# Kernel optimization log

Measured on AMD Instinct MI355X. Metric: run time of the kernel, lower is better.

## Reference

```python
import jax, jax.numpy as jnp
import numpy as np

N_NODES = 50000
N_EDGES = 600000
D_IN = 128
DIM = 128
N_REL = 3
N_LAYERS = 2


def setup_inputs() -> dict:
    key = jax.random.key(0)
    ks = jax.random.split(key, 10)
    s = 1.0 / np.sqrt(DIM)
    x = jax.random.normal(ks[0], (N_NODES, D_IN), dtype=jnp.float32)
    edge_index = jax.random.randint(ks[1], (2, N_EDGES), 0, N_NODES)
    edge_type = jax.random.randint(ks[2], (N_EDGES,), 0, N_REL)
    edge_weight = jax.random.uniform(ks[3], (N_EDGES,), dtype=jnp.float32)
    # stacked per-layer parameters (layer dims are uniform since D_IN == DIM)
    w_rel = jax.random.normal(ks[4], (N_LAYERS, N_REL, DIM, DIM), dtype=jnp.float32) * s
    w_root = jax.random.normal(ks[5], (N_LAYERS, DIM, DIM), dtype=jnp.float32) * s
    b_conv = jnp.zeros((N_LAYERS, DIM), dtype=jnp.float32)
    w_skip = jax.random.normal(ks[6], (N_LAYERS, D_IN, DIM), dtype=jnp.float32) * s
    b_skip = jnp.zeros((N_LAYERS, DIM), dtype=jnp.float32)
    return {"x": x, "edge_index": edge_index, "edge_type": edge_type,
            "edge_weight": edge_weight, "w_rel": w_rel, "w_root": w_root,
            "b_conv": b_conv, "w_skip": w_skip, "b_skip": b_skip}


def reference(x, edge_index, edge_type, edge_weight, w_rel, w_root, b_conv, w_skip, b_skip):
    n = x.shape[0]
    src, dst = edge_index[0], edge_index[1]
    h = x
    for l in range(w_rel.shape[0]):  # small fixed layer loop (2)
        skip = x @ w_skip[l] + b_skip[l]                      # [N, dim]
        # per-relation transform of all nodes: [R, N, dim] (cheap GEMMs),
        # avoids materializing a per-edge [E, d, d] weight gather
        hr = jnp.einsum('nd,rde->rne', h, w_rel[l])
        msgs = hr[edge_type, src] * edge_weight[:, None]      # [E, dim] gather
        agg = jax.ops.segment_sum(msgs, dst, num_segments=n)  # scatter-add
        h = agg + h @ w_root[l] + b_conv[l] + skip            # conv + skip residual
    return h
```

## Files before the change

### kernel.cpp

```cpp
#include <hip/hip_runtime.h>


#define DIM 128

typedef short short8 __attribute__((ext_vector_type(8)));
typedef float f32x4 __attribute__((ext_vector_type(4)));

__device__ __forceinline__ unsigned short f2bf(float f) {
    unsigned u = __float_as_uint(f);
    unsigned r = (u + 0x7FFFu + ((u >> 16) & 1u)) >> 16;
    return (unsigned short)r;
}
__device__ __forceinline__ float bflo(unsigned p) { return __uint_as_float(p << 16); }
__device__ __forceinline__ float bfhi(unsigned p) { return __uint_as_float(p & 0xFFFF0000u); }

__device__ __forceinline__ int xcc_id() {
    int x;
    asm volatile("s_getreg_b32 %0, hwreg(HW_REG_XCC_ID)" : "=s"(x));
    return x & 7;
}

__global__ void zero_kernel(int4* __restrict__ p, int n4) {
    int i = blockIdx.x * 256 + threadIdx.x;
    if (i < n4) p[i] = make_int4(0, 0, 0, 0);
}

#define K2_CONVB 2048
#define K2_PREPB 256
#define K2_CNTB  512

__device__ void conv_body(const float* __restrict__ in, unsigned short* __restrict__ ob,
                          int n8, int bid) {
    for (int i = bid * 256 + threadIdx.x; i < n8; i += K2_CONVB * 256) {
        const float4* ip = reinterpret_cast<const float4*>(in) + (size_t)i * 2;
        float4 v0 = ip[0], v1 = ip[1];
        uint4 o;
        o.x = (unsigned)f2bf(v0.x) | ((unsigned)f2bf(v0.y) << 16);
        o.y = (unsigned)f2bf(v0.z) | ((unsigned)f2bf(v0.w) << 16);
        o.z = (unsigned)f2bf(v1.x) | ((unsigned)f2bf(v1.y) << 16);
        o.w = (unsigned)f2bf(v1.z) | ((unsigned)f2bf(v1.w) << 16);
        reinterpret_cast<uint4*>(ob)[i] = o;
    }
}

__device__ void prep_body(const float* __restrict__ w_rel, const float* __restrict__ w_root,
                          const float* __restrict__ w_skip, unsigned short* __restrict__ WTf,
                          int bid) {
    for (int i = bid * 256 + threadIdx.x; i < 2 * 5 * DIM * DIM; i += K2_PREPB * 256) {
        int j    = i & 7;
        int lane = (i >> 3) & 63;
        int ks   = (i >> 9) & 3;
        int n    = (i >> 11) & 7;
        int s    = (i >> 14) % 5;
        int l    = i / (5 * DIM * DIM);
        int col = n * 16 + (lane & 15);
        int k   = ks * 32 + (lane >> 4) * 8 + j;
        float v;
        if (s < 3)       v = w_rel[(((size_t)l * 3 + s) * DIM + k) * DIM + col];
        else if (s == 3) {
            v = w_root[((size_t)l * DIM + k) * DIM + col];
            if (l == 0) v += w_skip[((size_t)k) * DIM + col];
        } else           v = w_skip[((size_t)l * DIM + k) * DIM + col];
        WTf[i] = f2bf(v);
    }
}

__device__ void count_body(const int* __restrict__ dst, int* __restrict__ counts8,
                           unsigned short* __restrict__ rank, int E, int N, int bid) {
    int* cp = counts8 + (size_t)xcc_id() * N;
    unsigned tag = (unsigned)xcc_id() << 13;
    int t = threadIdx.x;
    for (int base = bid * 1024; base < E; base += K2_CNTB * 1024) {
        int i0 = base + t, i1 = i0 + 256, i2 = i0 + 512, i3 = i0 + 768;
        int d0 = (i0 < E) ? dst[i0] : -1;
        int d1 = (i1 < E) ? dst[i1] : -1;
        int d2 = (i2 < E) ? dst[i2] : -1;
        int d3 = (i3 < E) ? dst[i3] : -1;
        int r0 = (d0 >= 0) ? atomicAdd(&cp[d0], 1) : 0;
        int r1 = (d1 >= 0) ? atomicAdd(&cp[d1], 1) : 0;
        int r2 = (d2 >= 0) ? atomicAdd(&cp[d2], 1) : 0;
        int r3 = (d3 >= 0) ? atomicAdd(&cp[d3], 1) : 0;
        if (d0 >= 0) rank[i0] = (unsigned short)(r0 | tag);
        if (d1 >= 0) rank[i1] = (unsigned short)(r1 | tag);
        if (d2 >= 0) rank[i2] = (unsigned short)(r2 | tag);
        if (d3 >= 0) rank[i3] = (unsigned short)(r3 | tag);
    }
}

__global__ __launch_bounds__(256) void fat_prep(
    const float* __restrict__ x, unsigned short* __restrict__ xb, int n8,
    const float* __restrict__ w_rel, const float* __restrict__ w_root,
    const float* __restrict__ w_skip, unsigned short* __restrict__ WTf,
    const int* __restrict__ dst, int* __restrict__ counts8,
    unsigned short* __restrict__ rank, int E, int N) {
    int b = blockIdx.x;
    if (b < K2_CONVB)                 conv_body(x, xb, n8, b);
    else if (b < K2_CONVB + K2_PREPB) prep_body(w_rel, w_root, w_skip, WTf, b - K2_CONVB);
    else                              count_body(dst, counts8, rank, E, N, b - K2_CONVB - K2_PREPB);
}

__global__ void bsum_kernel(const int* __restrict__ counts8, int* __restrict__ bsums, int n) {
    int t = threadIdx.x;
    int i = blockIdx.x * 256 + t;
    int v = 0;
    if (i < n) {
        #pragma unroll
        for (int p = 0; p < 8; ++p) v += counts8[(size_t)p * n + i];
    }
    for (int d = 32; d; d >>= 1) v += __shfl_down(v, d);
    __shared__ int ws[4];
    if ((t & 63) == 0) ws[t >> 6] = v;
    __syncthreads();
    if (t == 0) bsums[blockIdx.x] = ws[0] + ws[1] + ws[2] + ws[3];
}

__global__ void bscan_kernel(const int* __restrict__ bsums, int* __restrict__ bpre, int nblk) {
    __shared__ int s[256];
    int t = threadIdx.x;
    int v = (t < nblk) ? bsums[t] : 0;
    s[t] = v;
    __syncthreads();
    for (int d = 1; d < 256; d <<= 1) {
        int u = (t >= d) ? s[t - d] : 0;
        __syncthreads();
        s[t] += u;
        __syncthreads();
    }
    bpre[t] = s[t] - v;
}

__global__ void scan_final(const int* __restrict__ counts8, const int* __restrict__ bpre,
                           int* __restrict__ offsets, int* __restrict__ pos0,
                           int n, int E) {
    __shared__ int s[256];
    int t = threadIdx.x;
    int i = blockIdx.x * 256 + t;
    int c[8];
    int v = 0;
    if (i < n) {
        #pragma unroll
        for (int p = 0; p < 8; ++p) { c[p] = counts8[(size_t)p * n + i]; v += c[p]; }
    }
    s[t] = v;
    __syncthreads();
    for (int d = 1; d < 256; d <<= 1) {
        int u = (t >= d) ? s[t - d] : 0;
        __syncthreads();
        s[t] += u;
        __syncthreads();
    }
    int ex = s[t] - v + bpre[blockIdx.x];
    if (i < n) {
        offsets[i] = ex;
        int run = ex;
        #pragma unroll
        for (int p = 0; p < 8; ++p) { pos0[(size_t)p * n + i] = run; run += c[p]; }
    }
    if (i == 0) offsets[n] = E;
}

template<bool HAS_SKIP>
__device__ void gemm_body(
    int bid,
    const unsigned short* __restrict__ Ab, const unsigned short* __restrict__ Xb,
    const unsigned short* __restrict__ WTf,
    const float* __restrict__ bconv, const float* __restrict__ bskip,
    unsigned short* __restrict__ hr, void* __restrict__ outp, int M) {
    constexpr int NF = HAS_SKIP ? 40 : 32;
    __shared__ unsigned short stile[4][32][136];
    int t = threadIdx.x, lane = t & 63, wid = t >> 6;
    int lrow = lane & 15, lhi = lane >> 4;
    int r0 = bid * 128 + wid * 32;

    short8 af[2][4];
    #pragma unroll
    for (int rg = 0; rg < 2; ++rg) {
        int r = r0 + rg * 16 + lrow;
        const unsigned short* ap = Ab + (size_t)(r < M ? r : 0) * DIM + lhi * 8;
        #pragma unroll
        for (int ks = 0; ks < 4; ++ks)
            af[rg][ks] = *reinterpret_cast<const short8*>(ap + ks * 32);
    }
    short8 xf[2][4];
    f32x4 acc34[2][8];

    auto flush = [&](unsigned short* gbase) {
        #pragma unroll
        for (int j = 0; j < 8; ++j) {
            int lr = j * 4 + lhi;
            int lc = lrow * 8;
            int gr = r0 + lr;
            if (gr < M)
                *reinterpret_cast<uint4*>(gbase + (size_t)gr * DIM + lc) =
                    *reinterpret_cast<const uint4*>(&stile[wid][lr][lc]);
        }
    };

    short8 b0[4], b1[4];
    auto loadB = [&](int fi, short8* bb) {
        const unsigned short* p = WTf + ((size_t)fi * 4 * 64 + lane) * 8;
        #pragma unroll
        for (int ks = 0; ks < 4; ++ks)
            bb[ks] = *reinterpret_cast<const short8*>(p + ks * 512);
    };
    loadB(0, b0);
    #pragma unroll
    for (int fi = 0; fi < NF; ++fi) {
        short8* bc = (fi & 1) ? b1 : b0;
        short8* bn = (fi & 1) ? b0 : b1;
        if (fi + 1 < NF) loadB(fi + 1, bn);
        const int slot = fi >> 3, n = fi & 7;
        const int col = n * 16 + lrow;
        if (HAS_SKIP && slot == 3 && n == 0) {
            #pragma unroll
            for (int rg = 0; rg < 2; ++rg) {
                int r = r0 + rg * 16 + lrow;
                const unsigned short* xp = Xb + (size_t)(r < M ? r : 0) * DIM + lhi * 8;
                #pragma unroll
                for (int ks = 0; ks < 4; ++ks)
                    xf[rg][ks] = *reinterpret_cast<const short8*>(xp + ks * 32);
            }
        }
        if (slot < 3) {
            f32x4 a0 = {0.f, 0.f, 0.f, 0.f}, a1 = {0.f, 0.f, 0.f, 0.f};
            #pragma unroll
            for (int ks = 0; ks < 4; ++ks) {
                a0 = __builtin_amdgcn_mfma_f32_16x16x32_bf16(af[0][ks], bc[ks], a0, 0, 0, 0);
                a1 = __builtin_amdgcn_mfma_f32_16x16x32_bf16(af[1][ks], bc[ks], a1, 0, 0, 0);
            }
            #pragma unroll
            for (int rg = 0; rg < 2; ++rg) {
                f32x4& aa = rg ? a1 : a0;
                #pragma unroll
                for (int i2 = 0; i2 < 4; ++i2)
                    stile[wid][rg * 16 + lhi * 4 + i2][col] = f2bf(aa[i2]);
            }
            if (n == 7) flush(hr + (size_t)slot * M * DIM);
        } else if (!HAS_SKIP) {
            f32x4 a0 = {0.f, 0.f, 0.f, 0.f}, a1 = {0.f, 0.f, 0.f, 0.f};
            #pragma unroll
            for (int ks = 0; ks < 4; ++ks) {
                a0 = __builtin_amdgcn_mfma_f32_16x16x32_bf16(af[0][ks], bc[ks], a0, 0, 0, 0);
                a1 = __builtin_amdgcn_mfma_f32_16x16x32_bf16(af[1][ks], bc[ks], a1, 0, 0, 0);
            }
            float bb = bconv[col] + bskip[col];
            #pragma unroll
            for (int rg = 0; rg < 2; ++rg) {
                f32x4& aa = rg ? a1 : a0;
                #pragma unroll
                for (int i2 = 0; i2 < 4; ++i2)
                    stile[wid][rg * 16 + lhi * 4 + i2][col] = f2bf(aa[i2] + bb);
            }
            if (n == 7) flush((unsigned short*)outp);
        } else if (slot == 3) {
            f32x4 z = {0.f, 0.f, 0.f, 0.f};
            acc34[0][n] = z; acc34[1][n] = z;
            #pragma unroll
            for (int ks = 0; ks < 4; ++ks) {
                acc34[0][n] = __builtin_amdgcn_mfma_f32_16x16x32_bf16(af[0][ks], bc[ks], acc34[0][n], 0, 0, 0);
                acc34[1][n] = __builtin_amdgcn_mfma_f32_16x16x32_bf16(af[1][ks], bc[ks], acc34[1][n], 0, 0, 0);
            }
        } else {
            #pragma unroll
            for (int ks = 0; ks < 4; ++ks) {
                acc34[0][n] = __builtin_amdgcn_mfma_f32_16x16x32_bf16(xf[0][ks], bc[ks], acc34[0][n], 0, 0, 0);
                acc34[1][n] = __builtin_amdgcn_mfma_f32_16x16x32_bf16(xf[1][ks], bc[ks], acc34[1][n], 0, 0, 0);
            }
            float bb = bconv[col] + bskip[col];
            float* op = (float*)outp;
            #pragma unroll
            for (int rg = 0; rg < 2; ++rg) {
                #pragma unroll
                for (int i2 = 0; i2 < 4; ++i2) {
                    int r = r0 + rg * 16 + lhi * 4 + i2;
                    if (r < M) op[(size_t)r * DIM + col] = acc34[rg][n][i2] + bb;
                }
            }
        }
    }
}

#define K6_SCTB 512

__device__ void scatter_body(const int* __restrict__ src, const int* __restrict__ dst,
                             const int* __restrict__ etype, const float* __restrict__ ew,
                             const int* __restrict__ pos0,
                             const unsigned short* __restrict__ rank,
                             unsigned* __restrict__ csr, int E, int N, int bid) {
    for (int i = bid * 256 + threadIdx.x; i < E; i += K6_SCTB * 256) {
        int d = dst[i];
        unsigned rk = rank[i];
        int part = rk >> 13;
        int p = pos0[(size_t)part * N + d] + (rk & 0x1FFF);
        unsigned wq = (unsigned)__float2uint_rn(ew[i] * 16383.0f);
        csr[p] = (unsigned)src[i] | ((unsigned)etype[i] << 16) | (wq << 18);
    }
}

__global__ __launch_bounds__(256) void gemm0_scatter(
    const unsigned short* __restrict__ Ab, const unsigned short* __restrict__ WTf,
    const float* __restrict__ bconv, const float* __restrict__ bskip,
    unsigned short* __restrict__ hr, unsigned short* __restrict__ h1, int M, int GB,
    const int* __restrict__ src, const int* __restrict__ dst,
    const int* __restrict__ etype, const float* __restrict__ ew,
    const int* __restrict__ pos0, const unsigned short* __restrict__ rank,
    unsigned* __restrict__ csr, int E) {
    int b = blockIdx.x;
    if (b < GB) gemm_body<false>(b, Ab, nullptr, WTf, bconv, bskip, hr, h1, M);
    else        scatter_body(src, dst, etype, ew, pos0, rank, csr, E, M, b - GB);
}

__global__ __launch_bounds__(256) void gemm1_kernel(
    const unsigned short* __restrict__ Ab, const unsigned short* __restrict__ Xb,
    const unsigned short* __restrict__ WTf,
    const float* __restrict__ bconv, const float* __restrict__ bskip,
    unsigned short* __restrict__ hr, float* __restrict__ outp, int M) {
    gemm_body<true>(blockIdx.x, Ab, Xb, WTf, bconv, bskip, hr, outp, M);
}

template<bool BF16IO>
__global__ __launch_bounds__(256) void agg_kernel(
    const unsigned short* __restrict__ hr, const unsigned* __restrict__ csr,
    const int* __restrict__ offsets, float* __restrict__ outf,
    unsigned short* __restrict__ outb, int N) {
    int t = threadIdx.x;
    int lane = t & 63;
    int v = blockIdx.x * 4 + (t >> 6);
    if (v >= N) return;
    int g = lane >> 4;
    int l16 = lane & 15;
    int beg = offsets[v], end = offsets[v + 1];

    float acc[8] = {0.f, 0.f, 0.f, 0.f, 0.f, 0.f, 0.f, 0.f};
    int i = beg + g;
    bool valid = i < end;
    unsigned st = valid ? csr[i] : 0u;
    while (__any(valid)) {
        int ni = i + 4;
        bool nv = ni < end;
        unsigned nst = nv ? csr[ni] : 0u;
        if (valid) {
            int srcn = st & 0xFFFF;
            int rel  = (st >> 16) & 3;
            float w  = (float)(st >> 18) * (1.0f / 16383.0f);
            const unsigned short* row = hr + ((size_t)rel * N + srcn) * DIM + l16 * 8;
            uint4 pv = *reinterpret_cast<const uint4*>(row);
            acc[0] += w * bflo(pv.x); acc[1] += w * bfhi(pv.x);
            acc[2] += w * bflo(pv.y); acc[3] += w * bfhi(pv.y);
            acc[4] += w * bflo(pv.z); acc[5] += w * bfhi(pv.z);
            acc[6] += w * bflo(pv.w); acc[7] += w * bfhi(pv.w);
        }
        i = ni; st = nst; valid = nv;
    }
    #pragma unroll
    for (int j = 0; j < 8; ++j) {
        acc[j] += __shfl_xor(acc[j], 16);
        acc[j] += __shfl_xor(acc[j], 32);
    }
    if (g == 0) {
        if (BF16IO) {
            unsigned short* op = outb + (size_t)v * DIM + l16 * 8;
            uint4 cur = *reinterpret_cast<const uint4*>(op);
            float r0 = bflo(cur.x) + acc[0], r1 = bfhi(cur.x) + acc[1];
            float r2 = bflo(cur.y) + acc[2], r3 = bfhi(cur.y) + acc[3];
            float r4 = bflo(cur.z) + acc[4], r5 = bfhi(cur.z) + acc[5];
            float r6 = bflo(cur.w) + acc[6], r7 = bfhi(cur.w) + acc[7];
            uint4 o;
            o.x = (unsigned)f2bf(r0) | ((unsigned)f2bf(r1) << 16);
            o.y = (unsigned)f2bf(r2) | ((unsigned)f2bf(r3) << 16);
            o.z = (unsigned)f2bf(r4) | ((unsigned)f2bf(r5) << 16);
            o.w = (unsigned)f2bf(r6) | ((unsigned)f2bf(r7) << 16);
            *reinterpret_cast<uint4*>(op) = o;
        } else {
            float* op = outf + (size_t)v * DIM + l16 * 8;
            float4 c0 = *reinterpret_cast<float4*>(op);
            float4 c1 = *reinterpret_cast<float4*>(op + 4);
            c0.x += acc[0]; c0.y += acc[1]; c0.z += acc[2]; c0.w += acc[3];
            c1.x += acc[4]; c1.y += acc[5]; c1.z += acc[6]; c1.w += acc[7];
            *reinterpret_cast<float4*>(op) = c0;
            *reinterpret_cast<float4*>(op + 4) = c1;
        }
    }
}

extern "C" void kernel_launch(void* const* d_in, const int* in_sizes, int n_in,
                              void* d_out, int out_size, void* d_ws, size_t ws_size,
                              hipStream_t stream) {
    const float* x       = (const float*)d_in[0];
    const int*   eidx    = (const int*)d_in[1];
    const int*   etype   = (const int*)d_in[2];
    const float* ew      = (const float*)d_in[3];
    const float* w_rel   = (const float*)d_in[4];
    const float* w_root  = (const float*)d_in[5];
    const float* b_conv  = (const float*)d_in[6];
    const float* w_skip  = (const float*)d_in[7];
    const float* b_skip  = (const float*)d_in[8];

    const int N = in_sizes[0] / DIM;
    const int E = in_sizes[3];
    const int* src = eidx;
    const int* dst = eidx + E;
    const int nblk = (N + 255) / 256;

    char* w = (char*)d_ws;
    unsigned short* WTf  = (unsigned short*)w;  w += (size_t)2 * 5 * DIM * DIM * 2;
    unsigned short* xb   = (unsigned short*)w;  w += (size_t)N * DIM * 2;
    unsigned short* hr   = (unsigned short*)w;  w += (size_t)3 * N * DIM * 2;
    unsigned short* h1   = (unsigned short*)w;  w += (size_t)N * DIM * 2;
    int* counts8         = (int*)w;             w += (size_t)8 * N * 4;
    int* pos0            = (int*)w;             w += (size_t)8 * N * 4;
    int* offsets         = (int*)w;             w += (size_t)(N + 4) * 4;
    int* bsums           = (int*)w;             w += (size_t)256 * 4;
    int* bpre            = (int*)w;             w += (size_t)256 * 4;
    unsigned short* rank = (unsigned short*)w;  w += (size_t)E * 2;
    unsigned* csr        = (unsigned*)w;        w += (size_t)E * 4;

    float* out = (float*)d_out;

    const int n8 = N * DIM / 8;
    zero_kernel<<<(8 * N / 4 + 255) / 256, 256, 0, stream>>>((int4*)counts8, 8 * N / 4);
    fat_prep<<<K2_CONVB + K2_PREPB + K2_CNTB, 256, 0, stream>>>(
        x, xb, n8, w_rel, w_root, w_skip, WTf, dst, counts8, rank, E, N);
    bsum_kernel<<<nblk, 256, 0, stream>>>(counts8, bsums, N);
    bscan_kernel<<<1, 256, 0, stream>>>(bsums, bpre, nblk);
    scan_final<<<nblk, 256, 0, stream>>>(counts8, bpre, offsets, pos0, N, E);

    int GB = (N + 127) / 128;
    int ablocks = (N + 3) / 4;
    gemm0_scatter<<<GB + K6_SCTB, 256, 0, stream>>>(
        xb, WTf, b_conv, b_skip, hr, h1, N, GB,
        src, dst, etype, ew, pos0, rank, csr, E);
    agg_kernel<true><<<ablocks, 256, 0, stream>>>(hr, csr, offsets, nullptr, h1, N);
    gemm1_kernel<<<GB, 256, 0, stream>>>(h1, xb, WTf + (size_t)5 * DIM * DIM,
                                         b_conv + DIM, b_skip + DIM, hr, out, N);
    agg_kernel<false><<<ablocks, 256, 0, stream>>>(hr, csr, offsets, out, nullptr, N);
}
```

Before: 160.6 us.

## Aggregate before transform: gather raw features per relation, then GEMM

Reorders each layer so that neighbour features are first summed per relation into a [N,3,128] bf16 buffer, and the relation weights are applied afterwards in a GEMM. This replaces the old path, which wrote and then gathered a 3xN per-relation transformed array. The root and skip terms are folded into the same GEMM accumulators. Gathered rows shrink from hr to the plain feature array, which is more cache friendly, but the aggregation kernel now holds three accumulator sets and writes a 3x wider output, and one extra kernel launch is added. The fat_prep block order is also changed so the counting blocks run first.

```diff
diff --git a/kernel.cpp b/kernel.cpp
--- a/kernel.cpp
+++ b/kernel.cpp
@@ -13,6 +13,7 @@
 }
 __device__ __forceinline__ float bflo(unsigned p) { return __uint_as_float(p << 16); }
 __device__ __forceinline__ float bfhi(unsigned p) { return __uint_as_float(p & 0xFFFF0000u); }
+__device__ __forceinline__ float bfu(unsigned short u) { return __uint_as_float((unsigned)u << 16); }
 
 __device__ __forceinline__ int xcc_id() {
     int x;
@@ -25,9 +26,9 @@
     if (i < n4) p[i] = make_int4(0, 0, 0, 0);
 }
 
+#define K2_CNTB  512
+#define K2_PREPB 256
 #define K2_CONVB 2048
-#define K2_PREPB 256
-#define K2_CNTB  512
 
 __device__ void conv_body(const float* __restrict__ in, unsigned short* __restrict__ ob,
                           int n8, int bid) {
@@ -94,9 +95,9 @@
     const int* __restrict__ dst, int* __restrict__ counts8,
     unsigned short* __restrict__ rank, int E, int N) {
     int b = blockIdx.x;
-    if (b < K2_CONVB)                 conv_body(x, xb, n8, b);
-    else if (b < K2_CONVB + K2_PREPB) prep_body(w_rel, w_root, w_skip, WTf, b - K2_CONVB);
-    else                              count_body(dst, counts8, rank, E, N, b - K2_CONVB - K2_PREPB);
+    if (b < K2_CNTB)                 count_body(dst, counts8, rank, E, N, b);
+    else if (b < K2_CNTB + K2_PREPB) prep_body(w_rel, w_root, w_skip, WTf, b - K2_CNTB);
+    else                             conv_body(x, xb, n8, b - K2_CNTB - K2_PREPB);
 }
 
 __global__ void bsum_kernel(const int* __restrict__ counts8, int* __restrict__ bsums, int n) {
@@ -159,14 +160,10 @@
     if (i == 0) offsets[n] = E;
 }
 
-template<bool HAS_SKIP>
-__device__ void gemm_body(
-    int bid,
-    const unsigned short* __restrict__ Ab, const unsigned short* __restrict__ Xb,
-    const unsigned short* __restrict__ WTf,
-    const float* __restrict__ bconv, const float* __restrict__ bskip,
-    unsigned short* __restrict__ hr, void* __restrict__ outp, int M) {
-    constexpr int NF = HAS_SKIP ? 40 : 32;
+__device__ void root0_body(int bid, const unsigned short* __restrict__ xb,
+                           const unsigned short* __restrict__ WTf0,
+                           const float* __restrict__ bconv, const float* __restrict__ bskip,
+                           unsigned short* __restrict__ h1, int M) {
     __shared__ unsigned short stile[4][32][136];
     int t = threadIdx.x, lane = t & 63, wid = t >> 6;
     int lrow = lane & 15, lhi = lane >> 4;
@@ -176,107 +173,46 @@
     #pragma unroll
     for (int rg = 0; rg < 2; ++rg) {
         int r = r0 + rg * 16 + lrow;
-        const unsigned short* ap = Ab + (size_t)(r < M ? r : 0) * DIM + lhi * 8;
+        const unsigned short* ap = xb + (size_t)(r < M ? r : 0) * DIM + lhi * 8;
         #pragma unroll
         for (int ks = 0; ks < 4; ++ks)
             af[rg][ks] = *reinterpret_cast<const short8*>(ap + ks * 32);
     }
-    short8 xf[2][4];
-    f32x4 acc34[2][8];
-
-    auto flush = [&](unsigned short* gbase) {
-        #pragma unroll
-        for (int j = 0; j < 8; ++j) {
-            int lr = j * 4 + lhi;
-            int lc = lrow * 8;
-            int gr = r0 + lr;
-            if (gr < M)
-                *reinterpret_cast<uint4*>(gbase + (size_t)gr * DIM + lc) =
-                    *reinterpret_cast<const uint4*>(&stile[wid][lr][lc]);
-        }
-    };
-
     short8 b0[4], b1[4];
-    auto loadB = [&](int fi, short8* bb) {
-        const unsigned short* p = WTf + ((size_t)fi * 4 * 64 + lane) * 8;
+    auto loadB = [&](int fia, short8* bb) {
+        const unsigned short* p = WTf0 + ((size_t)fia * 256 + lane) * 8;
         #pragma unroll
         for (int ks = 0; ks < 4; ++ks)
             bb[ks] = *reinterpret_cast<const short8*>(p + ks * 512);
     };
-    loadB(0, b0);
-    #pragma unroll
-    for (int fi = 0; fi < NF; ++fi) {
-        short8* bc = (fi & 1) ? b1 : b0;
-        short8* bn = (fi & 1) ? b0 : b1;
-        if (fi + 1 < NF) loadB(fi + 1, bn);
-        const int slot = fi >> 3, n = fi & 7;
-        const int col = n * 16 + lrow;
-        if (HAS_SKIP && slot == 3 && n == 0) {
-            #pragma unroll
-            for (int rg = 0; rg < 2; ++rg) {
-                int r = r0 + rg * 16 + lrow;
-                const unsigned short* xp = Xb + (size_t)(r < M ? r : 0) * DIM + lhi * 8;
-                #pragma unroll
-                for (int ks = 0; ks < 4; ++ks)
-                    xf[rg][ks] = *reinterpret_cast<const short8*>(xp + ks * 32);
-            }
-        }
-        if (slot < 3) {
-            f32x4 a0 = {0.f, 0.f, 0.f, 0.f}, a1 = {0.f, 0.f, 0.f, 0.f};
-            #pragma unroll
-            for (int ks = 0; ks < 4; ++ks) {
-                a0 = __builtin_amdgcn_mfma_f32_16x16x32_bf16(af[0][ks], bc[ks], a0, 0, 0, 0);
-                a1 = __builtin_amdgcn_mfma_f32_16x16x32_bf16(af[1][ks], bc[ks], a1, 0, 0, 0);
-            }
-            #pragma unroll
-            for (int rg = 0; rg < 2; ++rg) {
-                f32x4& aa = rg ? a1 : a0;
-                #pragma unroll
-                for (int i2 = 0; i2 < 4; ++i2)
-                    stile[wid][rg * 16 + lhi * 4 + i2][col] = f2bf(aa[i2]);
-            }
-            if (n == 7) flush(hr + (size_t)slot * M * DIM);
-        } else if (!HAS_SKIP) {
-            f32x4 a0 = {0.f, 0.f, 0.f, 0.f}, a1 = {0.f, 0.f, 0.f, 0.f};
-            #pragma unroll
-            for (int ks = 0; ks < 4; ++ks) {
-                a0 = __builtin_amdgcn_mfma_f32_16x16x32_bf16(af[0][ks], bc[ks], a0, 0, 0, 0);
-                a1 = __builtin_amdgcn_mfma_f32_16x16x32_bf16(af[1][ks], bc[ks], a1, 0, 0, 0);
-            }
-            float bb = bconv[col] + bskip[col];
-            #pragma unroll
-            for (int rg = 0; rg < 2; ++rg) {
-                f32x4& aa = rg ? a1 : a0;
-                #pragma unroll
-                for (int i2 = 0; i2 < 4; ++i2)
-                    stile[wid][rg * 16 + lhi * 4 + i2][col] = f2bf(aa[i2] + bb);
-            }
-            if (n == 7) flush((unsigned short*)outp);
-        } else if (slot == 3) {
-            f32x4 z = {0.f, 0.f, 0.f, 0.f};
-            acc34[0][n] = z; acc34[1][n] = z;
-            #pragma unroll
-            for (int ks = 0; ks < 4; ++ks) {
-                acc34[0][n] = __builtin_amdgcn_mfma_f32_16x16x32_bf16(af[0][ks], bc[ks], acc34[0][n], 0, 0, 0);
-                acc34[1][n] = __builtin_amdgcn_mfma_f32_16x16x32_bf16(af[1][ks], bc[ks], acc34[1][n], 0, 0, 0);
-            }
-        } else {
-            #pragma unroll
-            for (int ks = 0; ks < 4; ++ks) {
-                acc34[0][n] = __builtin_amdgcn_mfma_f32_16x16x32_bf16(xf[0][ks], bc[ks], acc34[0][n], 0, 0, 0);
-                acc34[1][n] = __builtin_amdgcn_mfma_f32_16x16x32_bf16(xf[1][ks], bc[ks], acc34[1][n], 0, 0, 0);
-            }
-            float bb = bconv[col] + bskip[col];
-            float* op = (float*)outp;
-            #pragma unroll
-            for (int rg = 0; rg < 2; ++rg) {
-                #pragma unroll
-                for (int i2 = 0; i2 < 4; ++i2) {
-                    int r = r0 + rg * 16 + lhi * 4 + i2;
-                    if (r < M) op[(size_t)r * DIM + col] = acc34[rg][n][i2] + bb;
-                }
-            }
-        }
+    loadB(24, b0);
+    #pragma unroll
+    for (int n = 0; n < 8; ++n) {
+        short8* bc = (n & 1) ? b1 : b0;
+        short8* bn = (n & 1) ? b0 : b1;
+        if (n + 1 < 8) loadB(24 + n + 1, bn);
+        f32x4 a0 = {0.f, 0.f, 0.f, 0.f}, a1 = {0.f, 0.f, 0.f, 0.f};
+        #pragma unroll
+        for (int ks = 0; ks < 4; ++ks) {
+            a0 = __builtin_amdgcn_mfma_f32_16x16x32_bf16(af[0][ks], bc[ks], a0, 0, 0, 0);
+            a1 = __builtin_amdgcn_mfma_f32_16x16x32_bf16(af[1][ks], bc[ks], a1, 0, 0, 0);
+        }
+        int col = n * 16 + lrow;
+        float bb = bconv[col] + bskip[col];
+        #pragma unroll
+        for (int rg = 0; rg < 2; ++rg) {
+            f32x4& aa = rg ? a1 : a0;
+            #pragma unroll
+            for (int i2 = 0; i2 < 4; ++i2)
+                stile[wid][rg * 16 + lhi * 4 + i2][col] = f2bf(aa[i2] + bb);
+        }
+    }
+    #pragma unroll
+    for (int j = 0; j < 8; ++j) {
+        int lr = j * 4 + lhi, gr = r0 + lr;
+        if (gr < M)
+            *reinterpret_cast<uint4*>(h1 + (size_t)gr * DIM + lrow * 8) =
+                *reinterpret_cast<const uint4*>(&stile[wid][lr][lrow * 8]);
     }
 }
 
@@ -297,41 +233,29 @@
     }
 }
 
-__global__ __launch_bounds__(256) void gemm0_scatter(
-    const unsigned short* __restrict__ Ab, const unsigned short* __restrict__ WTf,
+__global__ __launch_bounds__(256) void fat2_root_scatter(
+    const unsigned short* __restrict__ xb, const unsigned short* __restrict__ WTf0,
     const float* __restrict__ bconv, const float* __restrict__ bskip,
-    unsigned short* __restrict__ hr, unsigned short* __restrict__ h1, int M, int GB,
+    unsigned short* __restrict__ h1, int M, int GB,
     const int* __restrict__ src, const int* __restrict__ dst,
     const int* __restrict__ etype, const float* __restrict__ ew,
     const int* __restrict__ pos0, const unsigned short* __restrict__ rank,
     unsigned* __restrict__ csr, int E) {
     int b = blockIdx.x;
-    if (b < GB) gemm_body<false>(b, Ab, nullptr, WTf, bconv, bskip, hr, h1, M);
+    if (b < GB) root0_body(b, xb, WTf0, bconv, bskip, h1, M);
     else        scatter_body(src, dst, etype, ew, pos0, rank, csr, E, M, b - GB);
 }
 
-__global__ __launch_bounds__(256) void gemm1_kernel(
-    const unsigned short* __restrict__ Ab, const unsigned short* __restrict__ Xb,
-    const unsigned short* __restrict__ WTf,
-    const float* __restrict__ bconv, const float* __restrict__ bskip,
-    unsigned short* __restrict__ hr, float* __restrict__ outp, int M) {
-    gemm_body<true>(blockIdx.x, Ab, Xb, WTf, bconv, bskip, hr, outp, M);
-}
-
-template<bool BF16IO>
-__global__ __launch_bounds__(256) void agg_kernel(
-    const unsigned short* __restrict__ hr, const unsigned* __restrict__ csr,
-    const int* __restrict__ offsets, float* __restrict__ outf,
-    unsigned short* __restrict__ outb, int N) {
-    int t = threadIdx.x;
-    int lane = t & 63;
+__global__ __launch_bounds__(256) void agg2_kernel(
+    const unsigned short* __restrict__ pool, const unsigned* __restrict__ csr,
+    const int* __restrict__ offsets, unsigned short* __restrict__ aggbuf, int N) {
+    int t = threadIdx.x, lane = t & 63;
     int v = blockIdx.x * 4 + (t >> 6);
     if (v >= N) return;
-    int g = lane >> 4;
-    int l16 = lane & 15;
+    int g = lane >> 4, l16 = lane & 15;
     int beg = offsets[v], end = offsets[v + 1];
 
-    float acc[8] = {0.f, 0.f, 0.f, 0.f, 0.f, 0.f, 0.f, 0.f};
+    float a0[8] = {0,0,0,0,0,0,0,0}, a1[8] = {0,0,0,0,0,0,0,0}, a2[8] = {0,0,0,0,0,0,0,0};
     int i = beg + g;
     bool valid = i < end;
     unsigned st = valid ? csr[i] : 0u;
@@ -343,42 +267,180 @@
             int srcn = st & 0xFFFF;
             int rel  = (st >> 16) & 3;
             float w  = (float)(st >> 18) * (1.0f / 16383.0f);
-            const unsigned short* row = hr + ((size_t)rel * N + srcn) * DIM + l16 * 8;
+            const unsigned short* row = pool + (size_t)srcn * DIM + l16 * 8;
             uint4 pv = *reinterpret_cast<const uint4*>(row);
-            acc[0] += w * bflo(pv.x); acc[1] += w * bfhi(pv.x);
-            acc[2] += w * bflo(pv.y); acc[3] += w * bfhi(pv.y);
-            acc[4] += w * bflo(pv.z); acc[5] += w * bfhi(pv.z);
-            acc[6] += w * bflo(pv.w); acc[7] += w * bfhi(pv.w);
+            float f[8];
+            f[0] = bflo(pv.x); f[1] = bfhi(pv.x); f[2] = bflo(pv.y); f[3] = bfhi(pv.y);
+            f[4] = bflo(pv.z); f[5] = bfhi(pv.z); f[6] = bflo(pv.w); f[7] = bfhi(pv.w);
+            float w0 = (rel == 0) ? w : 0.f;
+            float w1 = (rel == 1) ? w : 0.f;
+            float w2 = (rel == 2) ? w : 0.f;
+            #pragma unroll
+            for (int j = 0; j < 8; ++j) {
+                a0[j] += w0 * f[j];
+                a1[j] += w1 * f[j];
+                a2[j] += w2 * f[j];
+            }
         }
         i = ni; st = nst; valid = nv;
     }
     #pragma unroll
     for (int j = 0; j < 8; ++j) {
-        acc[j] += __shfl_xor(acc[j], 16);
-        acc[j] += __shfl_xor(acc[j], 32);
-    }
-    if (g == 0) {
-        if (BF16IO) {
-            unsigned short* op = outb + (size_t)v * DIM + l16 * 8;
-            uint4 cur = *reinterpret_cast<const uint4*>(op);
-            float r0 = bflo(cur.x) + acc[0], r1 = bfhi(cur.x) + acc[1];
-            float r2 = bflo(cur.y) + acc[2], r3 = bfhi(cur.y) + acc[3];
-            float r4 = bflo(cur.z) + acc[4], r5 = bfhi(cur.z) + acc[5];
-            float r6 = bflo(cur.w) + acc[6], r7 = bfhi(cur.w) + acc[7];
-            uint4 o;
-            o.x = (unsigned)f2bf(r0) | ((unsigned)f2bf(r1) << 16);
-            o.y = (unsigned)f2bf(r2) | ((unsigned)f2bf(r3) << 16);
-            o.z = (unsigned)f2bf(r4) | ((unsigned)f2bf(r5) << 16);
-            o.w = (unsigned)f2bf(r6) | ((unsigned)f2bf(r7) << 16);
-            *reinterpret_cast<uint4*>(op) = o;
-        } else {
-            float* op = outf + (size_t)v * DIM + l16 * 8;
-            float4 c0 = *reinterpret_cast<float4*>(op);
-            float4 c1 = *reinterpret_cast<float4*>(op + 4);
-            c0.x += acc[0]; c0.y += acc[1]; c0.z += acc[2]; c0.w += acc[3];
-            c1.x += acc[4]; c1.y += acc[5]; c1.z += acc[6]; c1.w += acc[7];
-            *reinterpret_cast<float4*>(op) = c0;
-            *reinterpret_cast<float4*>(op + 4) = c1;
+        a0[j] += __shfl_xor(a0[j], 16); a0[j] += __shfl_xor(a0[j], 32);
+        a1[j] += __shfl_xor(a1[j], 16); a1[j] += __shfl_xor(a1[j], 32);
+        a2[j] += __shfl_xor(a2[j], 16); a2[j] += __shfl_xor(a2[j], 32);
+    }
+    if (g < 3) {
+        float o[8];
+        #pragma unroll
+        for (int j = 0; j < 8; ++j)
+            o[j] = (g == 0) ? a0[j] : ((g == 1) ? a1[j] : a2[j]);
+        unsigned short* op = aggbuf + (size_t)v * 384 + g * 128 + l16 * 8;
+        uint4 w4;
+        w4.x = (unsigned)f2bf(o[0]) | ((unsigned)f2bf(o[1]) << 16);
+        w4.y = (unsigned)f2bf(o[2]) | ((unsigned)f2bf(o[3]) << 16);
+        w4.z = (unsigned)f2bf(o[4]) | ((unsigned)f2bf(o[5]) << 16);
+        w4.w = (unsigned)f2bf(o[6]) | ((unsigned)f2bf(o[7]) << 16);
+        *reinterpret_cast<uint4*>(op) = w4;
+    }
+}
+
+__global__ __launch_bounds__(256) void gemm0_kernel(
+    const unsigned short* __restrict__ aggbuf, const unsigned short* __restrict__ WTf0,
+    unsigned short* __restrict__ h1, int M) {
+    __shared__ unsigned short stile[4][32][136];
+    int bid = blockIdx.x;
+    int t = threadIdx.x, lane = t & 63, wid = t >> 6;
+    int lrow = lane & 15, lhi = lane >> 4;
+    int r0 = bid * 128 + wid * 32;
+
+    #pragma unroll
+    for (int j = 0; j < 8; ++j) {
+        int lr = j * 4 + lhi, gr = r0 + lr;
+        if (gr < M)
+            *reinterpret_cast<uint4*>(&stile[wid][lr][lrow * 8]) =
+                *reinterpret_cast<const uint4*>(h1 + (size_t)gr * DIM + lrow * 8);
+    }
+    f32x4 acc[2][8];
+    #pragma unroll
+    for (int rg = 0; rg < 2; ++rg)
+        #pragma unroll
+        for (int n = 0; n < 8; ++n)
+            #pragma unroll
+            for (int i2 = 0; i2 < 4; ++i2)
+                acc[rg][n][i2] = bfu(stile[wid][rg * 16 + lhi * 4 + i2][n * 16 + lrow]);
+
+    short8 af[2][4];
+    short8 b0[4], b1[4];
+    auto loadB = [&](int fia, short8* bb) {
+        const unsigned short* p = WTf0 + ((size_t)fia * 256 + lane) * 8;
+        #pragma unroll
+        for (int ks = 0; ks < 4; ++ks)
+            bb[ks] = *reinterpret_cast<const short8*>(p + ks * 512);
+    };
+    loadB(0, b0);
+    #pragma unroll
+    for (int fi = 0; fi < 24; ++fi) {
+        short8* bc = (fi & 1) ? b1 : b0;
+        short8* bn = (fi & 1) ? b0 : b1;
+        if (fi + 1 < 24) loadB(fi + 1, bn);
+        const int slot = fi >> 3, n = fi & 7;
+        if (n == 0) {
+            #pragma unroll
+            for (int rg = 0; rg < 2; ++rg) {
+                int r = r0 + rg * 16 + lrow;
+                const unsigned short* ap = aggbuf + (size_t)(r < M ? r : 0) * 384
+                                           + slot * 128 + lhi * 8;
+                #pragma unroll
+                for (int ks = 0; ks < 4; ++ks)
+                    af[rg][ks] = *reinterpret_cast<const short8*>(ap + ks * 32);
+            }
+        }
+        #pragma unroll
+        for (int ks = 0; ks < 4; ++ks) {
+            acc[0][n] = __builtin_amdgcn_mfma_f32_16x16x32_bf16(af[0][ks], bc[ks], acc[0][n], 0, 0, 0);
+            acc[1][n] = __builtin_amdgcn_mfma_f32_16x16x32_bf16(af[1][ks], bc[ks], acc[1][n], 0, 0, 0);
+        }
+    }
+    #pragma unroll
+    for (int rg = 0; rg < 2; ++rg)
+        #pragma unroll
+        for (int n = 0; n < 8; ++n)
+            #pragma unroll
+            for (int i2 = 0; i2 < 4; ++i2)
+                stile[wid][rg * 16 + lhi * 4 + i2][n * 16 + lrow] = f2bf(acc[rg][n][i2]);
+    #pragma unroll
+    for (int j = 0; j < 8; ++j) {
+        int lr = j * 4 + lhi, gr = r0 + lr;
+        if (gr < M)
+            *reinterpret_cast<uint4*>(h1 + (size_t)gr * DIM + lrow * 8) =
+                *reinterpret_cast<const uint4*>(&stile[wid][lr][lrow * 8]);
+    }
+}
+
+__global__ __launch_bounds__(256) void gemm1_kernel(
+    const unsigned short* __restrict__ aggbuf, const unsigned short* __restrict__ h1,
+    const unsigned short* __restrict__ xb, const unsigned short* __restrict__ WTf1,
+    const float* __restrict__ bconv, const float* __restrict__ bskip,
+    float* __restrict__ out, int M) {
+    int bid = blockIdx.x;
+    int t = threadIdx.x, lane = t & 63, wid = t >> 6;
+    int lrow = lane & 15, lhi = lane >> 4;
+    int r0 = bid * 128 + wid * 32;
+
+    f32x4 acc[2][8];
+    #pragma unroll
+    for (int rg = 0; rg < 2; ++rg)
+        #pragma unroll
+        for (int n = 0; n < 8; ++n)
+            acc[rg][n] = f32x4{0.f, 0.f, 0.f, 0.f};
+
+    short8 af[2][4];
+    short8 b0[4], b1[4];
+    auto loadB = [&](int fia, short8* bb) {
+        const unsigned short* p = WTf1 + ((size_t)fia * 256 + lane) * 8;
+        #pragma unroll
+        for (int ks = 0; ks < 4; ++ks)
+            bb[ks] = *reinterpret_cast<const short8*>(p + ks * 512);
+    };
+    loadB(0, b0);
+    #pragma unroll
+    for (int fi = 0; fi < 40; ++fi) {
+        short8* bc = (fi & 1) ? b1 : b0;
+        short8* bn = (fi & 1) ? b0 : b1;
+        if (fi + 1 < 40) loadB(fi + 1, bn);
+        const int slot = fi >> 3, n = fi & 7;
+        if (n == 0) {
+            #pragma unroll
+            for (int rg = 0; rg < 2; ++rg) {
+                int r = r0 + rg * 16 + lrow;
+                int rc = r < M ? r : 0;
+                const unsigned short* ap;
+                if (slot < 3)      ap = aggbuf + (size_t)rc * 384 + slot * 128 + lhi * 8;
+                else if (slot == 3) ap = h1 + (size_t)rc * DIM + lhi * 8;
+                else                ap = xb + (size_t)rc * DIM + lhi * 8;
+                #pragma unroll
+                for (int ks = 0; ks < 4; ++ks)
+                    af[rg][ks] = *reinterpret_cast<const short8*>(ap + ks * 32);
+            }
+        }
+        #pragma unroll
+        for (int ks = 0; ks < 4; ++ks) {
+            acc[0][n] = __builtin_amdgcn_mfma_f32_16x16x32_bf16(af[0][ks], bc[ks], acc[0][n], 0, 0, 0);
+            acc[1][n] = __builtin_amdgcn_mfma_f32_16x16x32_bf16(af[1][ks], bc[ks], acc[1][n], 0, 0, 0);
+        }
+    }
+    #pragma unroll
+    for (int n = 0; n < 8; ++n) {
+        int col = n * 16 + lrow;
+        float bb = bconv[col] + bskip[col];
+        #pragma unroll
+        for (int rg = 0; rg < 2; ++rg) {
+            #pragma unroll
+            for (int i2 = 0; i2 < 4; ++i2) {
+                int r = r0 + rg * 16 + lhi * 4 + i2;
+                if (r < M) out[(size_t)r * DIM + col] = acc[rg][n][i2] + bb;
+            }
         }
     }
 }
@@ -405,7 +467,7 @@
     char* w = (char*)d_ws;
     unsigned short* WTf  = (unsigned short*)w;  w += (size_t)2 * 5 * DIM * DIM * 2;
     unsigned short* xb   = (unsigned short*)w;  w += (size_t)N * DIM * 2;
-    unsigned short* hr   = (unsigned short*)w;  w += (size_t)3 * N * DIM * 2;
+    unsigned short* agg  = (unsigned short*)w;  w += (size_t)N * 3 * DIM * 2;
     unsigned short* h1   = (unsigned short*)w;  w += (size_t)N * DIM * 2;
     int* counts8         = (int*)w;             w += (size_t)8 * N * 4;
     int* pos0            = (int*)w;             w += (size_t)8 * N * 4;
@@ -416,10 +478,11 @@
     unsigned* csr        = (unsigned*)w;        w += (size_t)E * 4;
 
     float* out = (float*)d_out;
+    const unsigned short* WTf1 = WTf + (size_t)5 * DIM * DIM;
 
     const int n8 = N * DIM / 8;
     zero_kernel<<<(8 * N / 4 + 255) / 256, 256, 0, stream>>>((int4*)counts8, 8 * N / 4);
-    fat_prep<<<K2_CONVB + K2_PREPB + K2_CNTB, 256, 0, stream>>>(
+    fat_prep<<<K2_CNTB + K2_PREPB + K2_CONVB, 256, 0, stream>>>(
         x, xb, n8, w_rel, w_root, w_skip, WTf, dst, counts8, rank, E, N);
     bsum_kernel<<<nblk, 256, 0, stream>>>(counts8, bsums, N);
     bscan_kernel<<<1, 256, 0, stream>>>(bsums, bpre, nblk);
@@ -427,11 +490,12 @@
 
     int GB = (N + 127) / 128;
     int ablocks = (N + 3) / 4;
-    gemm0_scatter<<<GB + K6_SCTB, 256, 0, stream>>>(
-        xb, WTf, b_conv, b_skip, hr, h1, N, GB,
+    fat2_root_scatter<<<GB + K6_SCTB, 256, 0, stream>>>(
+        xb, WTf, b_conv, b_skip, h1, N, GB,
         src, dst, etype, ew, pos0, rank, csr, E);
-    agg_kernel<true><<<ablocks, 256, 0, stream>>>(hr, csr, offsets, nullptr, h1, N);
-    gemm1_kernel<<<GB, 256, 0, stream>>>(h1, xb, WTf + (size_t)5 * DIM * DIM,
-                                         b_conv + DIM, b_skip + DIM, hr, out, N);
-    agg_kernel<false><<<ablocks, 256, 0, stream>>>(hr, csr, offsets, out, nullptr, N);
-}
+    agg2_kernel<<<ablocks, 256, 0, stream>>>(xb, csr, offsets, agg, N);
+    gemm0_kernel<<<GB, 256, 0, stream>>>(agg, WTf, h1, N);
+    agg2_kernel<<<ablocks, 256, 0, stream>>>(h1, csr, offsets, agg, N);
+    gemm1_kernel<<<GB, 256, 0, stream>>>(agg, h1, xb, WTf1,
+                                         b_conv + DIM, b_skip + DIM, out, N);
+}
```

New measurement: 205.0 us. 1.28x slower.

## Replace rank-based CSR build with atomic cursor scatter and unroll aggregation loads

Applied to the files above, without the earlier changes.

Removes the per-edge rank array and per-XCC position table. The count kernel now only increments histograms, and the scatter pass claims CSR slots with atomicAdd on a per-node cursor. The count pass is split out of the fused prep kernel into its own launch. The aggregation loop now processes two edges per iteration with both row gathers issued before accumulation, which raises memory-level parallelism. The trade-off is more global atomics during scatter and a nondeterministic order within each CSR segment, which changes float summation order. It also adds one extra kernel launch.

```diff
diff --git a/kernel.cpp b/kernel.cpp
--- a/kernel.cpp
+++ b/kernel.cpp
@@ -27,7 +27,6 @@
 
 #define K2_CONVB 2048
 #define K2_PREPB 256
-#define K2_CNTB  512
 
 __device__ void conv_body(const float* __restrict__ in, unsigned short* __restrict__ ob,
                           int n8, int bid) {
@@ -65,38 +64,28 @@
     }
 }
 
-__device__ void count_body(const int* __restrict__ dst, int* __restrict__ counts8,
-                           unsigned short* __restrict__ rank, int E, int N, int bid) {
-    int* cp = counts8 + (size_t)xcc_id() * N;
-    unsigned tag = (unsigned)xcc_id() << 13;
-    int t = threadIdx.x;
-    for (int base = bid * 1024; base < E; base += K2_CNTB * 1024) {
-        int i0 = base + t, i1 = i0 + 256, i2 = i0 + 512, i3 = i0 + 768;
-        int d0 = (i0 < E) ? dst[i0] : -1;
-        int d1 = (i1 < E) ? dst[i1] : -1;
-        int d2 = (i2 < E) ? dst[i2] : -1;
-        int d3 = (i3 < E) ? dst[i3] : -1;
-        int r0 = (d0 >= 0) ? atomicAdd(&cp[d0], 1) : 0;
-        int r1 = (d1 >= 0) ? atomicAdd(&cp[d1], 1) : 0;
-        int r2 = (d2 >= 0) ? atomicAdd(&cp[d2], 1) : 0;
-        int r3 = (d3 >= 0) ? atomicAdd(&cp[d3], 1) : 0;
-        if (d0 >= 0) rank[i0] = (unsigned short)(r0 | tag);
-        if (d1 >= 0) rank[i1] = (unsigned short)(r1 | tag);
-        if (d2 >= 0) rank[i2] = (unsigned short)(r2 | tag);
-        if (d3 >= 0) rank[i3] = (unsigned short)(r3 | tag);
-    }
-}
-
-__global__ __launch_bounds__(256) void fat_prep(
+__global__ __launch_bounds__(256) void convprep_kernel(
     const float* __restrict__ x, unsigned short* __restrict__ xb, int n8,
     const float* __restrict__ w_rel, const float* __restrict__ w_root,
-    const float* __restrict__ w_skip, unsigned short* __restrict__ WTf,
-    const int* __restrict__ dst, int* __restrict__ counts8,
-    unsigned short* __restrict__ rank, int E, int N) {
+    const float* __restrict__ w_skip, unsigned short* __restrict__ WTf) {
     int b = blockIdx.x;
-    if (b < K2_CONVB)                 conv_body(x, xb, n8, b);
-    else if (b < K2_CONVB + K2_PREPB) prep_body(w_rel, w_root, w_skip, WTf, b - K2_CONVB);
-    else                              count_body(dst, counts8, rank, E, N, b - K2_CONVB - K2_PREPB);
+    if (b < K2_CONVB) conv_body(x, xb, n8, b);
+    else              prep_body(w_rel, w_root, w_skip, WTf, b - K2_CONVB);
+}
+
+#define K_CNTB 512
+
+__global__ __launch_bounds__(256) void count_kernel(
+    const int* __restrict__ dst, int* __restrict__ counts8, int E, int N) {
+    int* cp = counts8 + (size_t)xcc_id() * N;
+    int bid = blockIdx.x, t = threadIdx.x;
+    for (int base = bid * 1024; base < E; base += K_CNTB * 1024) {
+        int i0 = base + t, i1 = i0 + 256, i2 = i0 + 512, i3 = i0 + 768;
+        if (i0 < E) atomicAdd(&cp[dst[i0]], 1);
+        if (i1 < E) atomicAdd(&cp[dst[i1]], 1);
+        if (i2 < E) atomicAdd(&cp[dst[i2]], 1);
+        if (i3 < E) atomicAdd(&cp[dst[i3]], 1);
+    }
 }
 
 __global__ void bsum_kernel(const int* __restrict__ counts8, int* __restrict__ bsums, int n) {
@@ -130,16 +119,15 @@
 }
 
 __global__ void scan_final(const int* __restrict__ counts8, const int* __restrict__ bpre,
-                           int* __restrict__ offsets, int* __restrict__ pos0,
+                           int* __restrict__ offsets, int* __restrict__ cursor,
                            int n, int E) {
     __shared__ int s[256];
     int t = threadIdx.x;
     int i = blockIdx.x * 256 + t;
-    int c[8];
     int v = 0;
     if (i < n) {
         #pragma unroll
-        for (int p = 0; p < 8; ++p) { c[p] = counts8[(size_t)p * n + i]; v += c[p]; }
+        for (int p = 0; p < 8; ++p) v += counts8[(size_t)p * n + i];
     }
     s[t] = v;
     __syncthreads();
@@ -150,12 +138,7 @@
         __syncthreads();
     }
     int ex = s[t] - v + bpre[blockIdx.x];
-    if (i < n) {
-        offsets[i] = ex;
-        int run = ex;
-        #pragma unroll
-        for (int p = 0; p < 8; ++p) { pos0[(size_t)p * n + i] = run; run += c[p]; }
-    }
+    if (i < n) { offsets[i] = ex; cursor[i] = ex; }
     if (i == 0) offsets[n] = E;
 }
 
@@ -284,14 +267,11 @@
 
 __device__ void scatter_body(const int* __restrict__ src, const int* __restrict__ dst,
                              const int* __restrict__ etype, const float* __restrict__ ew,
-                             const int* __restrict__ pos0,
-                             const unsigned short* __restrict__ rank,
-                             unsigned* __restrict__ csr, int E, int N, int bid) {
+                             int* __restrict__ cursor,
+                             unsigned* __restrict__ csr, int E, int bid) {
     for (int i = bid * 256 + threadIdx.x; i < E; i += K6_SCTB * 256) {
         int d = dst[i];
-        unsigned rk = rank[i];
-        int part = rk >> 13;
-        int p = pos0[(size_t)part * N + d] + (rk & 0x1FFF);
+        int p = atomicAdd(&cursor[d], 1);
         unsigned wq = (unsigned)__float2uint_rn(ew[i] * 16383.0f);
         csr[p] = (unsigned)src[i] | ((unsigned)etype[i] << 16) | (wq << 18);
     }
@@ -303,11 +283,10 @@
     unsigned short* __restrict__ hr, unsigned short* __restrict__ h1, int M, int GB,
     const int* __restrict__ src, const int* __restrict__ dst,
     const int* __restrict__ etype, const float* __restrict__ ew,
-    const int* __restrict__ pos0, const unsigned short* __restrict__ rank,
-    unsigned* __restrict__ csr, int E) {
+    int* __restrict__ cursor, unsigned* __restrict__ csr, int E) {
     int b = blockIdx.x;
     if (b < GB) gemm_body<false>(b, Ab, nullptr, WTf, bconv, bskip, hr, h1, M);
-    else        scatter_body(src, dst, etype, ew, pos0, rank, csr, E, M, b - GB);
+    else        scatter_body(src, dst, etype, ew, cursor, csr, E, b - GB);
 }
 
 __global__ __launch_bounds__(256) void gemm1_kernel(
@@ -332,25 +311,39 @@
     int beg = offsets[v], end = offsets[v + 1];
 
     float acc[8] = {0.f, 0.f, 0.f, 0.f, 0.f, 0.f, 0.f, 0.f};
-    int i = beg + g;
-    bool valid = i < end;
-    unsigned st = valid ? csr[i] : 0u;
-    while (__any(valid)) {
-        int ni = i + 4;
-        bool nv = ni < end;
-        unsigned nst = nv ? csr[ni] : 0u;
-        if (valid) {
-            int srcn = st & 0xFFFF;
-            int rel  = (st >> 16) & 3;
-            float w  = (float)(st >> 18) * (1.0f / 16383.0f);
-            const unsigned short* row = hr + ((size_t)rel * N + srcn) * DIM + l16 * 8;
-            uint4 pv = *reinterpret_cast<const uint4*>(row);
-            acc[0] += w * bflo(pv.x); acc[1] += w * bfhi(pv.x);
-            acc[2] += w * bflo(pv.y); acc[3] += w * bfhi(pv.y);
-            acc[4] += w * bflo(pv.z); acc[5] += w * bfhi(pv.z);
-            acc[6] += w * bflo(pv.w); acc[7] += w * bfhi(pv.w);
-        }
-        i = ni; st = nst; valid = nv;
+    int iA = beg + g, iB = iA + 4;
+    bool vA = iA < end, vB = iB < end;
+    unsigned sA = vA ? csr[iA] : 0u;
+    unsigned sB = vB ? csr[iB] : 0u;
+    while (__any(vA)) {
+        uint4 pA = make_uint4(0, 0, 0, 0), pB = make_uint4(0, 0, 0, 0);
+        if (vA) {
+            const unsigned short* row = hr + ((size_t)((sA >> 16) & 3) * N + (sA & 0xFFFF)) * DIM + l16 * 8;
+            pA = *reinterpret_cast<const uint4*>(row);
+        }
+        if (vB) {
+            const unsigned short* row = hr + ((size_t)((sB >> 16) & 3) * N + (sB & 0xFFFF)) * DIM + l16 * 8;
+            pB = *reinterpret_cast<const uint4*>(row);
+        }
+        int nA = iA + 8, nB = iB + 8;
+        bool nvA = nA < end, nvB = nB < end;
+        unsigned nsA = nvA ? csr[nA] : 0u;
+        unsigned nsB = nvB ? csr[nB] : 0u;
+        if (vA) {
+            float w = (float)(sA >> 18) * (1.0f / 16383.0f);
+            acc[0] += w * bflo(pA.x); acc[1] += w * bfhi(pA.x);
+            acc[2] += w * bflo(pA.y); acc[3] += w * bfhi(pA.y);
+            acc[4] += w * bflo(pA.z); acc[5] += w * bfhi(pA.z);
+            acc[6] += w * bflo(pA.w); acc[7] += w * bfhi(pA.w);
+        }
+        if (vB) {
+            float w = (float)(sB >> 18) * (1.0f / 16383.0f);
+            acc[0] += w * bflo(pB.x); acc[1] += w * bfhi(pB.x);
+            acc[2] += w * bflo(pB.y); acc[3] += w * bfhi(pB.y);
+            acc[4] += w * bflo(pB.z); acc[5] += w * bfhi(pB.z);
+            acc[6] += w * bflo(pB.w); acc[7] += w * bfhi(pB.w);
+        }
+        iA = nA; iB = nB; sA = nsA; sB = nsB; vA = nvA; vB = nvB;
     }
     #pragma unroll
     for (int j = 0; j < 8; ++j) {
@@ -408,28 +401,28 @@
     unsigned short* hr   = (unsigned short*)w;  w += (size_t)3 * N * DIM * 2;
     unsigned short* h1   = (unsigned short*)w;  w += (size_t)N * DIM * 2;
     int* counts8         = (int*)w;             w += (size_t)8 * N * 4;
-    int* pos0            = (int*)w;             w += (size_t)8 * N * 4;
     int* offsets         = (int*)w;             w += (size_t)(N + 4) * 4;
+    int* cursor          = (int*)w;             w += (size_t)N * 4;
     int* bsums           = (int*)w;             w += (size_t)256 * 4;
     int* bpre            = (int*)w;             w += (size_t)256 * 4;
-    unsigned short* rank = (unsigned short*)w;  w += (size_t)E * 2;
     unsigned* csr        = (unsigned*)w;        w += (size_t)E * 4;
 
     float* out = (float*)d_out;
 
     const int n8 = N * DIM / 8;
     zero_kernel<<<(8 * N / 4 + 255) / 256, 256, 0, stream>>>((int4*)counts8, 8 * N / 4);
-    fat_prep<<<K2_CONVB + K2_PREPB + K2_CNTB, 256, 0, stream>>>(
-        x, xb, n8, w_rel, w_root, w_skip, WTf, dst, counts8, rank, E, N);
+    convprep_kernel<<<K2_CONVB + K2_PREPB, 256, 0, stream>>>(
+        x, xb, n8, w_rel, w_root, w_skip, WTf);
+    count_kernel<<<K_CNTB, 256, 0, stream>>>(dst, counts8, E, N);
     bsum_kernel<<<nblk, 256, 0, stream>>>(counts8, bsums, N);
     bscan_kernel<<<1, 256, 0, stream>>>(bsums, bpre, nblk);
-    scan_final<<<nblk, 256, 0, stream>>>(counts8, bpre, offsets, pos0, N, E);
+    scan_final<<<nblk, 256, 0, stream>>>(counts8, bpre, offsets, cursor, N, E);
 
     int GB = (N + 127) / 128;
     int ablocks = (N + 3) / 4;
     gemm0_scatter<<<GB + K6_SCTB, 256, 0, stream>>>(
         xb, WTf, b_conv, b_skip, hr, h1, N, GB,
-        src, dst, etype, ew, pos0, rank, csr, E);
+        src, dst, etype, ew, cursor, csr, E);
     agg_kernel<true><<<ablocks, 256, 0, stream>>>(hr, csr, offsets, nullptr, h1, N);
     gemm1_kernel<<<GB, 256, 0, stream>>>(h1, xb, WTf + (size_t)5 * DIM * DIM,
                                          b_conv + DIM, b_skip + DIM, hr, out, N);
```

Measured after the change: 178.2 us. 1.11x slower.
